# Kernel tuning notes

Measured on AMD Instinct MI355X. Metric: run time of the kernel, lower is better.

Reference implementation:

```python
import jax, jax.numpy as jnp
import numpy as np

N_NODES = 256
IN_FEATURES = 4096
OUT_FEATURES = 7
LAYERS = 4
WIRES = 8                      # ceil(log2(n_nodes))
DIM = 2 ** WIRES               # state-vector length = 256
P2 = WIRES * (WIRES - 1) // 2  # 28 controlled gates per block
N_W = 6 * WIRES + 3 * P2       # 132 weights per layer (matches weight_shape)
CPLX = jnp.complex64
# op2_all_layers ordering: gaps 1..w-1, then j
PAIRS = [(j, j + gap) for gap in range(1, WIRES) for j in range(WIRES - gap)]


def _ry(t):
    c, s = jnp.cos(t / 2), jnp.sin(t / 2)
    return jnp.stack([jnp.stack([c, -s]), jnp.stack([s, c])]).astype(CPLX)


def _rx(t):
    c = jnp.cos(t / 2).astype(CPLX)
    s = (-1j * jnp.sin(t / 2)).astype(CPLX)
    return jnp.stack([jnp.stack([c, s]), jnp.stack([s, c])])


def _rz(t):
    z = jnp.zeros((), CPLX)
    return jnp.stack([jnp.stack([jnp.exp(-0.5j * t).astype(CPLX), z]),
                      jnp.stack([z, jnp.exp(0.5j * t).astype(CPLX)])])


# Constant-angle gates (the source passes the integer weight index as the
# controlled-rotation angle, so these are compile-time numpy constants).
def _ry_np(a):
    c, s = np.cos(a / 2), np.sin(a / 2)
    return np.array([[c, -s], [s, c]], np.complex64)


def _rx_np(a):
    c, s = np.cos(a / 2), np.sin(a / 2)
    return np.array([[c, -1j * s], [-1j * s, c]], np.complex64)


def _rz_np(a):
    return np.diag([np.exp(-0.5j * a), np.exp(0.5j * a)]).astype(np.complex64)


def apply_1q(state, M, q):
    # state: [B] + [2]*WIRES; wire q lives on axis q+1 (wire 0 = MSB, PennyLane order)
    s = jnp.moveaxis(state, q + 1, -1)
    s = jnp.einsum('...b,ab->...a', s, M)
    return jnp.moveaxis(s, -1, q + 1)


def apply_c1q(state, M, c, t):
    # controlled gate: apply M on target wire t in the control==1 subspace
    s = jnp.moveaxis(state, (c + 1, t + 1), (-2, -1))
    s1 = jnp.einsum('...b,ab->...a', s[..., 1, :], M)
    s = jnp.stack([s[..., 0, :], s1], axis=-2)
    return jnp.moveaxis(s, (-2, -1), (c + 1, t + 1))


def q_layer(state, wv):
    # Faithful port of the source q_layer, including the quirk that the
    # CRY/CRX/CRZ angles are the integer running weight index (constants).
    wi = 0
    for q in range(WIRES):
        state = apply_1q(state, _ry(wv[wi + q]), q)
    wi += WIRES
    for i, (c, t) in enumerate(PAIRS):
        state = apply_c1q(state, _ry_np(float(wi + i)), c, t)
    wi += P2
    for q in range(WIRES):
        state = apply_1q(state, _ry(wv[wi + q]), q)
    wi += WIRES
    for q in range(WIRES):
        state = apply_1q(state, _rx(wv[wi + q]), q)
    wi += WIRES
    for i, (c, t) in enumerate(PAIRS):
        state = apply_c1q(state, _rx_np(float(wi + i)), c, t)
    wi += P2
    for q in range(WIRES):
        state = apply_1q(state, _rx(wv[wi + q]), q)
    wi += WIRES
    for q in range(WIRES):
        state = apply_1q(state, _rz(wv[wi + q]), q)
    wi += WIRES
    for i, (c, t) in enumerate(PAIRS):
        state = apply_c1q(state, _rz_np(float(wi + i)), c, t)
    wi += P2
    for q in range(WIRES):
        state = apply_1q(state, _rz(wv[wi + q]), q)
    return state


def circuit(samples, qweights):
    # samples: [B, N_NODES] real -> AmplitudeEmbedding(pad_with=0, normalize=True)
    B = samples.shape[0]
    v = samples
    if DIM > N_NODES:
        v = jnp.pad(v, ((0, 0), (0, DIM - N_NODES)))
    v = v / jnp.linalg.norm(v, axis=1, keepdims=True)
    state = v.astype(CPLX).reshape((B,) + (2,) * WIRES)
    layer = jax.checkpoint(q_layer)  # bounds residual memory under AD
    for l in range(LAYERS):
        state = layer(state, qweights[l])
    p = state.real ** 2 + state.imag ** 2  # probabilities, [B] + [2]*WIRES
    zs = []
    for q in range(WIRES):
        axes = tuple(a for a in range(1, WIRES + 1) if a != q + 1)
        m = p.sum(axis=axes)            # [B, 2]
        zs.append(m[:, 0] - m[:, 1])    # <Z_q> = P(0) - P(1)
    return jnp.stack(zs, axis=1)        # [B, WIRES]


def setup_inputs() -> dict:
    key = jax.random.key(0)
    k1, k2, k3, k4 = jax.random.split(key, 4)
    x = jax.random.normal(k1, (N_NODES, IN_FEATURES), jnp.float32)
    qweights = jax.random.uniform(k2, (LAYERS, N_W), jnp.float32, 0.0, 2.0 * np.pi)
    fc_w = jax.random.normal(k3, (OUT_FEATURES, WIRES), jnp.float32) / np.sqrt(WIRES)
    fc_b = jax.random.normal(k4, (OUT_FEATURES,), jnp.float32) / np.sqrt(WIRES)
    return {"x": x, "qweights": qweights, "fc_w": fc_w, "fc_b": fc_b}


def reference(x, qweights, fc_w, fc_b):
    z = circuit(x.T, qweights)      # [IN_FEATURES, WIRES]
    return z @ fc_w.T + fc_b        # [IN_FEATURES, OUT_FEATURES]
```

## Files before the change

kernel.cpp:

```cpp
#include <hip/hip_runtime.h>
#include <math.h>


namespace {

constexpr int NSAMP = 4096;
constexpr int NW_L  = 132;

constexpr double PI_D   = 3.14159265358979323846264338327950288;
constexpr double TWO_PI = 6.28318530717958647692528676655900577;

constexpr double red_pm_pi(double x) {
  double k = x / TWO_PI;
  long long ki = (long long)k;
  double r = x - (double)ki * TWO_PI;
  if (r > PI_D)  r -= TWO_PI;
  if (r < -PI_D) r += TWO_PI;
  return r;
}
constexpr double csin(double x) {
  double r = red_pm_pi(x), r2 = r * r, term = r, sum = r;
  for (int n = 1; n <= 13; ++n) { term *= -r2 / (double)((2*n)*(2*n+1)); sum += term; }
  return sum;
}
constexpr double ccos(double x) {
  double r = red_pm_pi(x), r2 = r * r, term = 1.0, sum = 1.0;
  for (int n = 1; n <= 13; ++n) { term *= -r2 / (double)((2*n-1)*(2*n)); sum += term; }
  return sum;
}

constexpr int PC[28] = {0,1,2,3,4,5,6, 0,1,2,3,4,5, 0,1,2,3,4, 0,1,2,3, 0,1,2, 0,1, 0};
constexpr int PT[28] = {1,2,3,4,5,6,7, 2,3,4,5,6,7, 3,4,5,6,7, 4,5,6,7, 5,6,7, 6,7, 7};

struct Tbl28 { float c[28]; float s[28]; };
constexpr Tbl28 mk_tbl(int base) {
  Tbl28 t{};
  for (int i = 0; i < 28; ++i) {
    double a = 0.5 * (double)(base + i);
    t.c[i] = (float)ccos(a);
    t.s[i] = (float)csin(a);
  }
  return t;
}
constexpr Tbl28 T_CRY = mk_tbl(8);
constexpr Tbl28 T_CRX = mk_tbl(52);

struct DTbl { float v[512]; };
constexpr DTbl mk_dcrz() {
  DTbl t{};
  for (int s = 0; s < 256; ++s) {
    double psi = 0.0;
    for (int i = 0; i < 28; ++i) {
      const int pc = 7 - PC[i], pt = 7 - PT[i];
      if ((s >> pc) & 1) {
        const double half = 0.5 * (double)(96 + i);
        psi += ((s >> pt) & 1) ? half : -half;
      }
    }
    t.v[2*s]   = (float)ccos(psi);
    t.v[2*s+1] = (float)csin(psi);
  }
  return t;
}
__device__ constexpr DTbl D_CRZ = mk_dcrz();

__device__ __forceinline__ float shx1(float v, int p) {
  if (p == 0) {
    int r = __builtin_amdgcn_update_dpp((int)__float_as_uint(v), (int)__float_as_uint(v),
                                        0xB1, 0xF, 0xF, true);
    return __uint_as_float((unsigned)r);
  }
  if (p == 1) {
    int r = __builtin_amdgcn_update_dpp((int)__float_as_uint(v), (int)__float_as_uint(v),
                                        0x4E, 0xF, 0xF, true);
    return __uint_as_float((unsigned)r);
  }
  if (p == 2) return __uint_as_float((unsigned)__builtin_amdgcn_ds_swizzle(
                      (int)__float_as_uint(v), 0x101F));
  if (p == 3) return __uint_as_float((unsigned)__builtin_amdgcn_ds_swizzle(
                      (int)__float_as_uint(v), 0x201F));
  if (p == 4) return __uint_as_float((unsigned)__builtin_amdgcn_ds_swizzle(
                      (int)__float_as_uint(v), 0x401F));
  return __shfl_xor(v, 32, 64);
}

__device__ __forceinline__ void gen_lane(float& ar, float& ai, int s, int p,
                                         float m00r, float m00i, float m01r, float m01i) {
  const int b = (s >> p) & 1;
  const float dr = m00r;
  const float di = b ? -m00i : m00i;
  const float g  = b ? -m01r : m01r;
  const float hh = m01i;
  const float pr = shx1(ar, p);
  const float pi = shx1(ai, p);
  const float mr = ar, mi = ai;
  ar = dr*mr - di*mi + g*pr - hh*pi;
  ai = dr*mi + di*mr + g*pi + hh*pr;
}
__device__ __forceinline__ void gen_xw(float& ar, float& ai, int s, int p,
                                       float m00r, float m00i, float m01r, float m01i,
                                       float2* xbuf) {
  xbuf[s] = make_float2(ar, ai);
  __syncthreads();
  const float2 pt = xbuf[s ^ (1 << p)];
  __syncthreads();
  const int b = (s >> p) & 1;
  const float dr = m00r;
  const float di = b ? -m00i : m00i;
  const float g  = b ? -m01r : m01r;
  const float hh = m01i;
  const float mr = ar, mi = ai;
  ar = dr*mr - di*mi + g*pt.x - hh*pt.y;
  ai = dr*mi + di*mr + g*pt.y + hh*pt.x;
}
__device__ __forceinline__ void cry_lane(float& ar, float& ai, int s, int pc, int pt,
                                         float cc, float sc) {
  const int ctrl = (s >> pc) & 1;
  const float ce = ctrl ? cc : 1.0f;
  float se = ((s >> pt) & 1) ? sc : -sc;
  se = ctrl ? se : 0.0f;
  const float pr = shx1(ar, pt);
  const float pi = shx1(ai, pt);
  ar = ce*ar + se*pr;
  ai = ce*ai + se*pi;
}
__device__ __forceinline__ void cry_xw(float& ar, float& ai, int s, int pc, int pt,
                                       float cc, float sc, float2* xbuf) {
  xbuf[s] = make_float2(ar, ai);
  __syncthreads();
  const float2 p = xbuf[s ^ (1 << pt)];
  __syncthreads();
  const int ctrl = (s >> pc) & 1;
  const float ce = ctrl ? cc : 1.0f;
  float se = ((s >> pt) & 1) ? sc : -sc;
  se = ctrl ? se : 0.0f;
  ar = ce*ar + se*p.x;
  ai = ce*ai + se*p.y;
}
__device__ __forceinline__ void crx_lane(float& ar, float& ai, int s, int pc, int pt,
                                         float cc, float sc) {
  const int ctrl = (s >> pc) & 1;
  const float ce = ctrl ? cc : 1.0f;
  const float se = ctrl ? sc : 0.0f;
  const float pr = shx1(ar, pt);
  const float pi = shx1(ai, pt);
  ar = ce*ar + se*pi;
  ai = ce*ai - se*pr;
}
__device__ __forceinline__ void crx_xw(float& ar, float& ai, int s, int pc, int pt,
                                       float cc, float sc, float2* xbuf) {
  xbuf[s] = make_float2(ar, ai);
  __syncthreads();
  const float2 p = xbuf[s ^ (1 << pt)];
  __syncthreads();
  const int ctrl = (s >> pc) & 1;
  const float ce = ctrl ? cc : 1.0f;
  const float se = ctrl ? sc : 0.0f;
  ar = ce*ar + se*p.y;
  ai = ce*ai - se*p.x;
}

__device__ __forceinline__ unsigned short f2bf(float f) {
  unsigned int u = __float_as_uint(f);
  u = (u + 0x7FFFu + ((u >> 16) & 1u)) >> 16;
  return (unsigned short)u;
}

typedef __attribute__((ext_vector_type(8))) short bf16x8;
typedef __attribute__((ext_vector_type(4))) float f32x4;

}

__global__ __launch_bounds__(256) void build_half4w(const float* __restrict__ qw,
                                                    float* __restrict__ U1c,
                                                    float* __restrict__ U2c) {
  __shared__ float4 sM[48];
  __shared__ float2 xbuf[256];
  const int tid = threadIdx.x;
  const int h   = blockIdx.x >> 8;
  const int s0  = blockIdx.x & 255;
  const int s   = tid;

  if (tid < 48) {
    const int lp  = tid / 24;
    const int rem = tid - lp * 24;
    const int j   = rem >> 3;
    const int q   = rem & 7;
    const int l   = 2 * h + lp;
    float a, bb;
    if (j == 0) {
      a  = qw[l * NW_L + q];
      bb = (l > 0) ? qw[(l - 1) * NW_L + 124 + q] : 0.f;
    } else if (j == 1) {
      a  = qw[l * NW_L + 44 + q];
      bb = qw[l * NW_L + 36 + q];
    } else {
      a  = (l < 3) ? qw[l * NW_L + 88 + q] : 0.f;
      bb = qw[l * NW_L + 80 + q];
    }
    float sa, ca, sb, cb;
    __sincosf(0.5f * a,  &sa, &ca);
    __sincosf(0.5f * bb, &sb, &cb);
    float4 m;
    if (j == 0)      m = make_float4(ca*cb, -ca*sb, -sa*cb, -sa*sb);
    else if (j == 1) m = make_float4(ca*cb, -sa*sb, -ca*sb, -sa*cb);
    else             m = make_float4(ca*cb, -sa*cb, -sb*sa, -sb*ca);
    sM[tid] = m;
  }

  float ar = (s == s0) ? 1.f : 0.f;
  float ai = 0.f;
  const float dzr = D_CRZ.v[2*s];
  const float dzi = D_CRZ.v[2*s+1];
  __syncthreads();

#pragma unroll 1
  for (int lp = 0; lp < 2; ++lp) {
    const int base = lp * 24;
#pragma unroll
    for (int q = 0; q < 8; ++q) {
      float4 m = sM[base + q];
      if (q == 0)      gen_xw(ar, ai, s, 7, m.x, m.y, m.z, m.w, xbuf);
      else if (q == 1) gen_xw(ar, ai, s, 6, m.x, m.y, m.z, m.w, xbuf);
      else             gen_lane(ar, ai, s, 7 - q, m.x, m.y, m.z, m.w);
    }
#pragma unroll
    for (int i = 0; i < 28; ++i) {
      const int pc = 7 - PC[i], pt = 7 - PT[i];
      const float cc = T_CRY.c[i], sc = T_CRY.s[i];
      if (pt == 6) cry_xw(ar, ai, s, pc, pt, cc, sc, xbuf);
      else         cry_lane(ar, ai, s, pc, pt, cc, sc);
    }
#pragma unroll
    for (int q = 0; q < 8; ++q) {
      float4 m = sM[base + 8 + q];
      if (q == 0)      gen_xw(ar, ai, s, 7, m.x, m.y, m.z, m.w, xbuf);
      else if (q == 1) gen_xw(ar, ai, s, 6, m.x, m.y, m.z, m.w, xbuf);
      else             gen_lane(ar, ai, s, 7 - q, m.x, m.y, m.z, m.w);
    }
#pragma unroll
    for (int i = 0; i < 28; ++i) {
      const int pc = 7 - PC[i], pt = 7 - PT[i];
      const float cc = T_CRX.c[i], sc = T_CRX.s[i];
      if (pt == 6) crx_xw(ar, ai, s, pc, pt, cc, sc, xbuf);
      else         crx_lane(ar, ai, s, pc, pt, cc, sc);
    }
#pragma unroll
    for (int q = 0; q < 8; ++q) {
      float4 m = sM[base + 16 + q];
      if (q == 0)      gen_xw(ar, ai, s, 7, m.x, m.y, m.z, m.w, xbuf);
      else if (q == 1) gen_xw(ar, ai, s, 6, m.x, m.y, m.z, m.w, xbuf);
      else             gen_lane(ar, ai, s, 7 - q, m.x, m.y, m.z, m.w);
    }
    if (2 * h + lp < 3) {
      const float mr = ar, mi = ai;
      ar = mr*dzr - mi*dzi;
      ai = mr*dzi + mi*dzr;
    }
  }

  float* Uc = h ? U2c : U1c;
  ((float2*)(Uc + (size_t)s0 * 512))[s] = make_float2(ar, ai);
}

__global__ __launch_bounds__(256) void combine_u(const float* __restrict__ U1c,
                                                 const float* __restrict__ U2c,
                                                 unsigned short* __restrict__ Ubf) {
  __shared__ float2 S2[32 * 16];
  __shared__ float2 S1[16 * 33];
  const int tid = threadIdx.x;
  const int ti  = tid & 15;
  const int tj  = tid >> 4;
  const int bi  = blockIdx.x & 15;
  const int bj  = blockIdx.x >> 4;

  float accr = 0.f, acci = 0.f;
#pragma unroll 1
  for (int kt = 0; kt < 8; ++kt) {
    __syncthreads();
#pragma unroll
    for (int v = 0; v < 2; ++v) {
      const int s = v * 256 + tid;
      const int k  = s >> 4, i = s & 15;
      S2[k * 16 + i] = *(const float2*)(U2c + (size_t)(kt*32 + k) * 512 + (bi*16 + i) * 2);
      const int j2 = s >> 5, k2 = s & 31;
      S1[j2 * 33 + k2] = *(const float2*)(U1c + (size_t)(bj*16 + j2) * 512 + (kt*32 + k2) * 2);
    }
    __syncthreads();
#pragma unroll
    for (int kk = 0; kk < 32; ++kk) {
      const float2 a = S2[kk * 16 + ti];
      const float2 b = S1[tj * 33 + kk];
      accr = fmaf(a.x, b.x, accr);  accr = fmaf(-a.y, b.y, accr);
      acci = fmaf(a.x, b.y, acci);  acci = fmaf(a.y, b.x, acci);
    }
  }
  const int i = bi * 16 + ti, j = bj * 16 + tj;
  Ubf[(size_t)i * 256 + j]         = f2bf(accr);
  Ubf[(size_t)(i + 256) * 256 + j] = f2bf(acci);
}

__global__ __launch_bounds__(1024) void eval3(const float* __restrict__ x,
                                              const unsigned short* __restrict__ Ubf,
                                              const float* __restrict__ fcw,
                                              const float* __restrict__ fcb,
                                              float* __restrict__ out) {
  __shared__ unsigned short Xs[16 * 264];
  __shared__ float Zp[16][16][9];
  __shared__ float Zf[16][9];
  const int tid  = threadIdx.x;
  const int lane = tid & 63;
  const int w    = tid >> 6;
  const int colbase = blockIdx.x * 16;

  {
    const int k  = tid >> 2;
    const int c4 = (tid & 3) * 4;
    const float4 v = *(const float4*)(x + (size_t)k * NSAMP + colbase + c4);
    Xs[(c4 + 0) * 264 + k] = f2bf(v.x);
    Xs[(c4 + 1) * 264 + k] = f2bf(v.y);
    Xs[(c4 + 2) * 264 + k] = f2bf(v.z);
    Xs[(c4 + 3) * 264 + k] = f2bf(v.w);
  }
  __syncthreads();

  const int quad = lane >> 4;
  const int n    = lane & 15;
  const int rowb = w * 32;

  f32x4 acc[2];
  acc[0] = (f32x4){0.f, 0.f, 0.f, 0.f};
  acc[1] = (f32x4){0.f, 0.f, 0.f, 0.f};

#pragma unroll
  for (int kt = 0; kt < 8; ++kt) {
    const bf16x8 bfrag = *(const bf16x8*)&Xs[n * 264 + kt * 32 + quad * 8];
#pragma unroll
    for (int rt = 0; rt < 2; ++rt) {
      const int row = rowb + rt * 16 + n;
      const bf16x8 afrag = *(const bf16x8*)(Ubf + (size_t)row * 256 + kt * 32 + quad * 8);
      acc[rt] = __builtin_amdgcn_mfma_f32_16x16x32_bf16(afrag, bfrag, acc[rt], 0, 0, 0);
    }
  }

  float za[9];
#pragma unroll
  for (int i = 0; i < 9; ++i) za[i] = 0.f;
  const float m4 = (lane & 32) ? -1.f : 1.f;
  const float m5 = (lane & 16) ? -1.f : 1.f;
#pragma unroll
  for (int rt = 0; rt < 2; ++rt) {
#pragma unroll
    for (int reg = 0; reg < 4; ++reg) {
      const float v = acc[rt][reg];
      const float p = v * v;
      za[0] += p;
      za[1] += (w & 4)   ? -p : p;
      za[2] += (w & 2)   ? -p : p;
      za[3] += (w & 1)   ? -p : p;
      za[4] += rt        ? -p : p;
      za[5] = fmaf(m4, p, za[5]);
      za[6] = fmaf(m5, p, za[6]);
      za[7] += (reg & 2) ? -p : p;
      za[8] += (reg & 1) ? -p : p;
    }
  }
#pragma unroll
  for (int off = 16; off <= 32; off <<= 1) {
#pragma unroll
    for (int i = 0; i < 9; ++i) za[i] += __shfl_xor(za[i], off, 64);
  }
  if (lane < 16) {
#pragma unroll
    for (int i = 0; i < 9; ++i) Zp[w][lane][i] = za[i];
  }
  __syncthreads();

  if (tid < 144) {
    const int col = tid / 9, q = tid - col * 9;
    float z = 0.f;
#pragma unroll
    for (int ww = 0; ww < 16; ++ww) z += Zp[ww][col][q];
    Zf[col][q] = z;
  }
  __syncthreads();

  if (tid < 112) {
    const int col = tid / 7, oo = tid - col * 7;
    const float inv = 1.f / Zf[col][0];
    float v = fcb[oo];
#pragma unroll
    for (int q = 0; q < 8; ++q)
      v = fmaf(fcw[oo * 8 + q], Zf[col][1 + q] * inv, v);
    out[(size_t)(colbase + col) * 7 + oo] = v;
  }
}

extern "C" void kernel_launch(void* const* d_in, const int* in_sizes, int n_in,
                              void* d_out, int out_size, void* d_ws, size_t ws_size,
                              hipStream_t stream) {
  const float* x   = (const float*)d_in[0];
  const float* qw  = (const float*)d_in[1];
  const float* fcw = (const float*)d_in[2];
  const float* fcb = (const float*)d_in[3];
  float* out = (float*)d_out;

  float* U1c = (float*)d_ws;
  float* U2c = U1c + 256 * 512;
  unsigned short* Ubf = (unsigned short*)(U2c + 256 * 512);

  hipLaunchKernelGGL(build_half4w, dim3(512), dim3(256),  0, stream, qw, U1c, U2c);
  hipLaunchKernelGGL(combine_u,    dim3(256), dim3(256),  0, stream, U1c, U2c, Ubf);
  hipLaunchKernelGGL(eval3,        dim3(256), dim3(1024), 0, stream, x, Ubf, fcw, fcb, out);
}
```

Before: 89.28 us.

## Drop unitary-combine kernel by chaining two half-circuit GEMMs in eval

Instead of forming the full circuit unitary with a separate complex matmul kernel, the build kernel now produces rows of each half-circuit directly, using an inverse-circuit trick to get rows instead of columns, and writes them in bf16 as a real-packed complex matrix. The eval kernel then applies the first half via MFMA, stages the bf16 intermediate in shared memory, and applies the second half as a 512x512 real block GEMM. This removes one kernel launch and the fp32 combine pass, at the cost of roughly three times the MFMA work per eval block and an extra bf16 rounding of the intermediate state.

```diff
diff --git a/kernel.cpp b/kernel.cpp
--- a/kernel.cpp
+++ b/kernel.cpp
@@ -171,14 +171,14 @@
 
 }
 
-__global__ __launch_bounds__(256) void build_half4w(const float* __restrict__ qw,
-                                                    float* __restrict__ U1c,
-                                                    float* __restrict__ U2c) {
+__global__ __launch_bounds__(256) void build_rows4w(const float* __restrict__ qw,
+                                                    unsigned short* __restrict__ U1bf,
+                                                    unsigned short* __restrict__ W2bf) {
   __shared__ float4 sM[48];
   __shared__ float2 xbuf[256];
   const int tid = threadIdx.x;
   const int h   = blockIdx.x >> 8;
-  const int s0  = blockIdx.x & 255;
+  const int o   = blockIdx.x & 255;
   const int s   = tid;
 
   if (tid < 48) {
@@ -208,104 +208,78 @@
     sM[tid] = m;
   }
 
-  float ar = (s == s0) ? 1.f : 0.f;
+  float ar = (s == o) ? 1.f : 0.f;
   float ai = 0.f;
-  const float dzr = D_CRZ.v[2*s];
-  const float dzi = D_CRZ.v[2*s+1];
+  const float dzr =  D_CRZ.v[2*s];
+  const float dzi = -D_CRZ.v[2*s+1];
   __syncthreads();
 
 #pragma unroll 1
-  for (int lp = 0; lp < 2; ++lp) {
+  for (int lp = 1; lp >= 0; --lp) {
+    const int l    = 2 * h + lp;
     const int base = lp * 24;
-#pragma unroll
-    for (int q = 0; q < 8; ++q) {
-      float4 m = sM[base + q];
-      if (q == 0)      gen_xw(ar, ai, s, 7, m.x, m.y, m.z, m.w, xbuf);
-      else if (q == 1) gen_xw(ar, ai, s, 6, m.x, m.y, m.z, m.w, xbuf);
-      else             gen_lane(ar, ai, s, 7 - q, m.x, m.y, m.z, m.w);
-    }
-#pragma unroll
-    for (int i = 0; i < 28; ++i) {
-      const int pc = 7 - PC[i], pt = 7 - PT[i];
-      const float cc = T_CRY.c[i], sc = T_CRY.s[i];
-      if (pt == 6) cry_xw(ar, ai, s, pc, pt, cc, sc, xbuf);
-      else         cry_lane(ar, ai, s, pc, pt, cc, sc);
-    }
-#pragma unroll
-    for (int q = 0; q < 8; ++q) {
-      float4 m = sM[base + 8 + q];
-      if (q == 0)      gen_xw(ar, ai, s, 7, m.x, m.y, m.z, m.w, xbuf);
-      else if (q == 1) gen_xw(ar, ai, s, 6, m.x, m.y, m.z, m.w, xbuf);
-      else             gen_lane(ar, ai, s, 7 - q, m.x, m.y, m.z, m.w);
-    }
-#pragma unroll
-    for (int i = 0; i < 28; ++i) {
-      const int pc = 7 - PC[i], pt = 7 - PT[i];
-      const float cc = T_CRX.c[i], sc = T_CRX.s[i];
-      if (pt == 6) crx_xw(ar, ai, s, pc, pt, cc, sc, xbuf);
-      else         crx_lane(ar, ai, s, pc, pt, cc, sc);
-    }
-#pragma unroll
-    for (int q = 0; q < 8; ++q) {
-      float4 m = sM[base + 16 + q];
-      if (q == 0)      gen_xw(ar, ai, s, 7, m.x, m.y, m.z, m.w, xbuf);
-      else if (q == 1) gen_xw(ar, ai, s, 6, m.x, m.y, m.z, m.w, xbuf);
-      else             gen_lane(ar, ai, s, 7 - q, m.x, m.y, m.z, m.w);
-    }
-    if (2 * h + lp < 3) {
+    if (l < 3) {
       const float mr = ar, mi = ai;
       ar = mr*dzr - mi*dzi;
       ai = mr*dzi + mi*dzr;
     }
-  }
-
-  float* Uc = h ? U2c : U1c;
-  ((float2*)(Uc + (size_t)s0 * 512))[s] = make_float2(ar, ai);
-}
-
-__global__ __launch_bounds__(256) void combine_u(const float* __restrict__ U1c,
-                                                 const float* __restrict__ U2c,
-                                                 unsigned short* __restrict__ Ubf) {
-  __shared__ float2 S2[32 * 16];
-  __shared__ float2 S1[16 * 33];
-  const int tid = threadIdx.x;
-  const int ti  = tid & 15;
-  const int tj  = tid >> 4;
-  const int bi  = blockIdx.x & 15;
-  const int bj  = blockIdx.x >> 4;
-
-  float accr = 0.f, acci = 0.f;
-#pragma unroll 1
-  for (int kt = 0; kt < 8; ++kt) {
-    __syncthreads();
-#pragma unroll
-    for (int v = 0; v < 2; ++v) {
-      const int s = v * 256 + tid;
-      const int k  = s >> 4, i = s & 15;
-      S2[k * 16 + i] = *(const float2*)(U2c + (size_t)(kt*32 + k) * 512 + (bi*16 + i) * 2);
-      const int j2 = s >> 5, k2 = s & 31;
-      S1[j2 * 33 + k2] = *(const float2*)(U1c + (size_t)(bj*16 + j2) * 512 + (kt*32 + k2) * 2);
-    }
-    __syncthreads();
-#pragma unroll
-    for (int kk = 0; kk < 32; ++kk) {
-      const float2 a = S2[kk * 16 + ti];
-      const float2 b = S1[tj * 33 + kk];
-      accr = fmaf(a.x, b.x, accr);  accr = fmaf(-a.y, b.y, accr);
-      acci = fmaf(a.x, b.y, acci);  acci = fmaf(a.y, b.x, acci);
-    }
-  }
-  const int i = bi * 16 + ti, j = bj * 16 + tj;
-  Ubf[(size_t)i * 256 + j]         = f2bf(accr);
-  Ubf[(size_t)(i + 256) * 256 + j] = f2bf(acci);
-}
-
-__global__ __launch_bounds__(1024) void eval3(const float* __restrict__ x,
-                                              const unsigned short* __restrict__ Ubf,
-                                              const float* __restrict__ fcw,
-                                              const float* __restrict__ fcb,
-                                              float* __restrict__ out) {
+#pragma unroll
+    for (int q = 0; q < 8; ++q) {
+      float4 m = sM[base + 16 + q];
+      if (q == 0)      gen_xw(ar, ai, s, 7, m.x, -m.y, -m.z, -m.w, xbuf);
+      else if (q == 1) gen_xw(ar, ai, s, 6, m.x, -m.y, -m.z, -m.w, xbuf);
+      else             gen_lane(ar, ai, s, 7 - q, m.x, -m.y, -m.z, -m.w);
+    }
+#pragma unroll
+    for (int i = 27; i >= 0; --i) {
+      const int pc = 7 - PC[i], pt = 7 - PT[i];
+      const float cc = T_CRX.c[i], sc = -T_CRX.s[i];
+      if (pt == 6) crx_xw(ar, ai, s, pc, pt, cc, sc, xbuf);
+      else         crx_lane(ar, ai, s, pc, pt, cc, sc);
+    }
+#pragma unroll
+    for (int q = 0; q < 8; ++q) {
+      float4 m = sM[base + 8 + q];
+      if (q == 0)      gen_xw(ar, ai, s, 7, m.x, -m.y, -m.z, -m.w, xbuf);
+      else if (q == 1) gen_xw(ar, ai, s, 6, m.x, -m.y, -m.z, -m.w, xbuf);
+      else             gen_lane(ar, ai, s, 7 - q, m.x, -m.y, -m.z, -m.w);
+    }
+#pragma unroll
+    for (int i = 27; i >= 0; --i) {
+      const int pc = 7 - PC[i], pt = 7 - PT[i];
+      const float cc = T_CRY.c[i], sc = -T_CRY.s[i];
+      if (pt == 6) cry_xw(ar, ai, s, pc, pt, cc, sc, xbuf);
+      else         cry_lane(ar, ai, s, pc, pt, cc, sc);
+    }
+#pragma unroll
+    for (int q = 0; q < 8; ++q) {
+      float4 m = sM[base + q];
+      if (q == 0)      gen_xw(ar, ai, s, 7, m.x, -m.y, -m.z, -m.w, xbuf);
+      else if (q == 1) gen_xw(ar, ai, s, 6, m.x, -m.y, -m.z, -m.w, xbuf);
+      else             gen_lane(ar, ai, s, 7 - q, m.x, -m.y, -m.z, -m.w);
+    }
+  }
+
+  if (h == 0) {
+    U1bf[(size_t)o * 256 + s]         = f2bf(ar);
+    U1bf[(size_t)(o + 256) * 256 + s] = f2bf(-ai);
+  } else {
+    U1bf += 0;
+    W2bf[(size_t)o * 512 + s]               = f2bf(ar);
+    W2bf[(size_t)o * 512 + 256 + s]         = f2bf(ai);
+    W2bf[(size_t)(o + 256) * 512 + s]       = f2bf(-ai);
+    W2bf[(size_t)(o + 256) * 512 + 256 + s] = f2bf(ar);
+  }
+}
+
+__global__ __launch_bounds__(1024) void eval_chain(const float* __restrict__ x,
+                                                   const unsigned short* __restrict__ U1bf,
+                                                   const unsigned short* __restrict__ W2bf,
+                                                   const float* __restrict__ fcw,
+                                                   const float* __restrict__ fcb,
+                                                   float* __restrict__ out) {
   __shared__ unsigned short Xs[16 * 264];
+  __shared__ unsigned short Ys[16 * 520];
   __shared__ float Zp[16][16][9];
   __shared__ float Zf[16][9];
   const int tid  = threadIdx.x;
@@ -328,17 +302,40 @@
   const int n    = lane & 15;
   const int rowb = w * 32;
 
+  {
+    f32x4 a1[2];
+    a1[0] = (f32x4){0.f, 0.f, 0.f, 0.f};
+    a1[1] = (f32x4){0.f, 0.f, 0.f, 0.f};
+#pragma unroll
+    for (int kt = 0; kt < 8; ++kt) {
+      const bf16x8 bfrag = *(const bf16x8*)&Xs[n * 264 + kt * 32 + quad * 8];
+#pragma unroll
+      for (int rt = 0; rt < 2; ++rt) {
+        const int row = rowb + rt * 16 + n;
+        const bf16x8 afrag = *(const bf16x8*)(U1bf + (size_t)row * 256 + kt * 32 + quad * 8);
+        a1[rt] = __builtin_amdgcn_mfma_f32_16x16x32_bf16(afrag, bfrag, a1[rt], 0, 0, 0);
+      }
+    }
+#pragma unroll
+    for (int rt = 0; rt < 2; ++rt) {
+      unsigned short p4[4];
+#pragma unroll
+      for (int reg = 0; reg < 4; ++reg) p4[reg] = f2bf(a1[rt][reg]);
+      *(uint2*)&Ys[n * 520 + rowb + rt * 16 + quad * 4] = *(const uint2*)p4;
+    }
+  }
+  __syncthreads();
+
   f32x4 acc[2];
   acc[0] = (f32x4){0.f, 0.f, 0.f, 0.f};
   acc[1] = (f32x4){0.f, 0.f, 0.f, 0.f};
-
-#pragma unroll
-  for (int kt = 0; kt < 8; ++kt) {
-    const bf16x8 bfrag = *(const bf16x8*)&Xs[n * 264 + kt * 32 + quad * 8];
+#pragma unroll
+  for (int kt = 0; kt < 16; ++kt) {
+    const bf16x8 bfrag = *(const bf16x8*)&Ys[n * 520 + kt * 32 + quad * 8];
 #pragma unroll
     for (int rt = 0; rt < 2; ++rt) {
       const int row = rowb + rt * 16 + n;
-      const bf16x8 afrag = *(const bf16x8*)(Ubf + (size_t)row * 256 + kt * 32 + quad * 8);
+      const bf16x8 afrag = *(const bf16x8*)(W2bf + (size_t)row * 512 + kt * 32 + quad * 8);
       acc[rt] = __builtin_amdgcn_mfma_f32_16x16x32_bf16(afrag, bfrag, acc[rt], 0, 0, 0);
     }
   }
@@ -405,11 +402,10 @@
   const float* fcb = (const float*)d_in[3];
   float* out = (float*)d_out;
 
-  float* U1c = (float*)d_ws;
-  float* U2c = U1c + 256 * 512;
-  unsigned short* Ubf = (unsigned short*)(U2c + 256 * 512);
-
-  hipLaunchKernelGGL(build_half4w, dim3(512), dim3(256),  0, stream, qw, U1c, U2c);
-  hipLaunchKernelGGL(combine_u,    dim3(256), dim3(256),  0, stream, U1c, U2c, Ubf);
-  hipLaunchKernelGGL(eval3,        dim3(256), dim3(1024), 0, stream, x, Ubf, fcw, fcb, out);
-}
+  unsigned short* U1bf = (unsigned short*)d_ws;
+  unsigned short* W2bf = U1bf + (size_t)512 * 256;
+
+  hipLaunchKernelGGL(build_rows4w, dim3(512), dim3(256),  0, stream, qw, U1bf, W2bf);
+  hipLaunchKernelGGL(eval_chain,   dim3(256), dim3(1024), 0, stream,
+                     x, U1bf, W2bf, fcw, fcb, out);
+}
```

Measured after the change: 94.60 us. +6.0%, slower.

## Split unitary build into per-layer quarters and chain two GEMMs in eval

Applied to the files above, without the earlier changes.

The circuit unitary is now built one layer per block, across four times as many blocks with half the serial gate depth each. The combine kernel now forms two two-layer products, U1 = L1·L0 and U2 = L3·L2, instead of one four-layer product. U1 is stored as a stacked real/imag bf16 matrix, and U2 as a 512x512 real-block matrix [[Re,-Im],[Im,Re]]. The eval kernel then does two chained MFMA GEMMs (U1·x, then W2·y) with the intermediate in shared memory. This shortens the serial critical path of the build stage, at the cost of more eval-stage MFMA work, roughly tripling its matmul FLOPs, and an extra bf16 rounding of the intermediate state.

```diff
diff --git a/kernel.cpp b/kernel.cpp
--- a/kernel.cpp
+++ b/kernel.cpp
@@ -169,24 +169,50 @@
 typedef __attribute__((ext_vector_type(8))) short bf16x8;
 typedef __attribute__((ext_vector_type(4))) float f32x4;
 
-}
-
-__global__ __launch_bounds__(256) void build_half4w(const float* __restrict__ qw,
-                                                    float* __restrict__ U1c,
-                                                    float* __restrict__ U2c) {
-  __shared__ float4 sM[48];
+__device__ __forceinline__ void cgemm_tile(const float* __restrict__ bufA,
+                                           const float* __restrict__ bufB,
+                                           int bi, int bj, int tid,
+                                           float& accr, float& acci,
+                                           float2* S2 , float2* S1 ) {
+  const int ti = tid & 15;
+  const int tj = tid >> 4;
+  accr = 0.f; acci = 0.f;
+#pragma unroll 1
+  for (int kt = 0; kt < 8; ++kt) {
+    __syncthreads();
+#pragma unroll
+    for (int v = 0; v < 2; ++v) {
+      const int s = v * 256 + tid;
+      const int k = s >> 4, i = s & 15;
+      S2[k * 16 + i] = *(const float2*)(bufA + (size_t)(kt*32 + k) * 512 + (bi*16 + i) * 2);
+      const int j2 = s >> 5, k2 = s & 31;
+      S1[j2 * 33 + k2] = *(const float2*)(bufB + (size_t)(bj*16 + j2) * 512 + (kt*32 + k2) * 2);
+    }
+    __syncthreads();
+#pragma unroll
+    for (int kk = 0; kk < 32; ++kk) {
+      const float2 a = S2[kk * 16 + ti];
+      const float2 b = S1[tj * 33 + kk];
+      accr = fmaf(a.x, b.x, accr);  accr = fmaf(-a.y, b.y, accr);
+      acci = fmaf(a.x, b.y, acci);  acci = fmaf(a.y, b.x, acci);
+    }
+  }
+}
+
+}
+
+__global__ __launch_bounds__(256) void build_quarter4w(const float* __restrict__ qw,
+                                                       float* __restrict__ Uq) {
+  __shared__ float4 sM[24];
   __shared__ float2 xbuf[256];
   const int tid = threadIdx.x;
-  const int h   = blockIdx.x >> 8;
+  const int l   = blockIdx.x >> 8;
   const int s0  = blockIdx.x & 255;
   const int s   = tid;
 
-  if (tid < 48) {
-    const int lp  = tid / 24;
-    const int rem = tid - lp * 24;
-    const int j   = rem >> 3;
-    const int q   = rem & 7;
-    const int l   = 2 * h + lp;
+  if (tid < 24) {
+    const int j = tid >> 3;
+    const int q = tid & 7;
     float a, bb;
     if (j == 0) {
       a  = qw[l * NW_L + q];
@@ -214,98 +240,105 @@
   const float dzi = D_CRZ.v[2*s+1];
   __syncthreads();
 
-#pragma unroll 1
-  for (int lp = 0; lp < 2; ++lp) {
-    const int base = lp * 24;
-#pragma unroll
-    for (int q = 0; q < 8; ++q) {
-      float4 m = sM[base + q];
-      if (q == 0)      gen_xw(ar, ai, s, 7, m.x, m.y, m.z, m.w, xbuf);
-      else if (q == 1) gen_xw(ar, ai, s, 6, m.x, m.y, m.z, m.w, xbuf);
-      else             gen_lane(ar, ai, s, 7 - q, m.x, m.y, m.z, m.w);
-    }
-#pragma unroll
-    for (int i = 0; i < 28; ++i) {
-      const int pc = 7 - PC[i], pt = 7 - PT[i];
-      const float cc = T_CRY.c[i], sc = T_CRY.s[i];
-      if (pt == 6) cry_xw(ar, ai, s, pc, pt, cc, sc, xbuf);
-      else         cry_lane(ar, ai, s, pc, pt, cc, sc);
-    }
-#pragma unroll
-    for (int q = 0; q < 8; ++q) {
-      float4 m = sM[base + 8 + q];
-      if (q == 0)      gen_xw(ar, ai, s, 7, m.x, m.y, m.z, m.w, xbuf);
-      else if (q == 1) gen_xw(ar, ai, s, 6, m.x, m.y, m.z, m.w, xbuf);
-      else             gen_lane(ar, ai, s, 7 - q, m.x, m.y, m.z, m.w);
-    }
-#pragma unroll
-    for (int i = 0; i < 28; ++i) {
-      const int pc = 7 - PC[i], pt = 7 - PT[i];
-      const float cc = T_CRX.c[i], sc = T_CRX.s[i];
-      if (pt == 6) crx_xw(ar, ai, s, pc, pt, cc, sc, xbuf);
-      else         crx_lane(ar, ai, s, pc, pt, cc, sc);
-    }
-#pragma unroll
-    for (int q = 0; q < 8; ++q) {
-      float4 m = sM[base + 16 + q];
-      if (q == 0)      gen_xw(ar, ai, s, 7, m.x, m.y, m.z, m.w, xbuf);
-      else if (q == 1) gen_xw(ar, ai, s, 6, m.x, m.y, m.z, m.w, xbuf);
-      else             gen_lane(ar, ai, s, 7 - q, m.x, m.y, m.z, m.w);
-    }
-    if (2 * h + lp < 3) {
-      const float mr = ar, mi = ai;
-      ar = mr*dzr - mi*dzi;
-      ai = mr*dzi + mi*dzr;
-    }
-  }
-
-  float* Uc = h ? U2c : U1c;
-  ((float2*)(Uc + (size_t)s0 * 512))[s] = make_float2(ar, ai);
-}
-
-__global__ __launch_bounds__(256) void combine_u(const float* __restrict__ U1c,
-                                                 const float* __restrict__ U2c,
-                                                 unsigned short* __restrict__ Ubf) {
+#pragma unroll
+  for (int q = 0; q < 8; ++q) {
+    float4 m = sM[q];
+    if (q == 0)      gen_xw(ar, ai, s, 7, m.x, m.y, m.z, m.w, xbuf);
+    else if (q == 1) gen_xw(ar, ai, s, 6, m.x, m.y, m.z, m.w, xbuf);
+    else             gen_lane(ar, ai, s, 7 - q, m.x, m.y, m.z, m.w);
+  }
+#pragma unroll
+  for (int i = 0; i < 28; ++i) {
+    const int pc = 7 - PC[i], pt = 7 - PT[i];
+    const float cc = T_CRY.c[i], sc = T_CRY.s[i];
+    if (pt == 6) cry_xw(ar, ai, s, pc, pt, cc, sc, xbuf);
+    else         cry_lane(ar, ai, s, pc, pt, cc, sc);
+  }
+#pragma unroll
+  for (int q = 0; q < 8; ++q) {
+    float4 m = sM[8 + q];
+    if (q == 0)      gen_xw(ar, ai, s, 7, m.x, m.y, m.z, m.w, xbuf);
+    else if (q == 1) gen_xw(ar, ai, s, 6, m.x, m.y, m.z, m.w, xbuf);
+    else             gen_lane(ar, ai, s, 7 - q, m.x, m.y, m.z, m.w);
+  }
+#pragma unroll
+  for (int i = 0; i < 28; ++i) {
+    const int pc = 7 - PC[i], pt = 7 - PT[i];
+    const float cc = T_CRX.c[i], sc = T_CRX.s[i];
+    if (pt == 6) crx_xw(ar, ai, s, pc, pt, cc, sc, xbuf);
+    else         crx_lane(ar, ai, s, pc, pt, cc, sc);
+  }
+#pragma unroll
+  for (int q = 0; q < 8; ++q) {
+    float4 m = sM[16 + q];
+    if (q == 0)      gen_xw(ar, ai, s, 7, m.x, m.y, m.z, m.w, xbuf);
+    else if (q == 1) gen_xw(ar, ai, s, 6, m.x, m.y, m.z, m.w, xbuf);
+    else             gen_lane(ar, ai, s, 7 - q, m.x, m.y, m.z, m.w);
+  }
+  if (l < 3) {
+    const float mr = ar, mi = ai;
+    ar = mr*dzr - mi*dzi;
+    ai = mr*dzi + mi*dzr;
+  }
+
+  ((float2*)(Uq + (size_t)(l * 256 + s0) * 512))[s] = make_float2(ar, ai);
+}
+
+__global__ __launch_bounds__(256) void combine_emit(const float* __restrict__ Uq,
+                                                    unsigned short* __restrict__ U1bf,
+                                                    unsigned short* __restrict__ W2bf) {
   __shared__ float2 S2[32 * 16];
   __shared__ float2 S1[16 * 33];
+  __shared__ float Tre[16][17];
+  __shared__ float Tim[16][17];
   const int tid = threadIdx.x;
-  const int ti  = tid & 15;
-  const int tj  = tid >> 4;
-  const int bi  = blockIdx.x & 15;
-  const int bj  = blockIdx.x >> 4;
-
-  float accr = 0.f, acci = 0.f;
-#pragma unroll 1
-  for (int kt = 0; kt < 8; ++kt) {
-    __syncthreads();
-#pragma unroll
-    for (int v = 0; v < 2; ++v) {
-      const int s = v * 256 + tid;
-      const int k  = s >> 4, i = s & 15;
-      S2[k * 16 + i] = *(const float2*)(U2c + (size_t)(kt*32 + k) * 512 + (bi*16 + i) * 2);
-      const int j2 = s >> 5, k2 = s & 31;
-      S1[j2 * 33 + k2] = *(const float2*)(U1c + (size_t)(bj*16 + j2) * 512 + (kt*32 + k2) * 2);
-    }
-    __syncthreads();
-#pragma unroll
-    for (int kk = 0; kk < 32; ++kk) {
-      const float2 a = S2[kk * 16 + ti];
-      const float2 b = S1[tj * 33 + kk];
-      accr = fmaf(a.x, b.x, accr);  accr = fmaf(-a.y, b.y, accr);
-      acci = fmaf(a.x, b.y, acci);  acci = fmaf(a.y, b.x, acci);
-    }
-  }
-  const int i = bi * 16 + ti, j = bj * 16 + tj;
-  Ubf[(size_t)i * 256 + j]         = f2bf(accr);
-  Ubf[(size_t)(i + 256) * 256 + j] = f2bf(acci);
-}
-
-__global__ __launch_bounds__(1024) void eval3(const float* __restrict__ x,
-                                              const unsigned short* __restrict__ Ubf,
-                                              const float* __restrict__ fcw,
-                                              const float* __restrict__ fcb,
-                                              float* __restrict__ out) {
+  const int p   = blockIdx.x >> 8;
+  const int rem = blockIdx.x & 255;
+  const int bi  = rem & 15;
+  const int bj  = rem >> 4;
+  const float* bufA = Uq + (size_t)(2*p + 1) * 256 * 512;
+  const float* bufB = Uq + (size_t)(2*p) * 256 * 512;
+
+  float accr, acci;
+  cgemm_tile(bufA, bufB, bi, bj, tid, accr, acci, S2, S1);
+
+  Tre[tid & 15][tid >> 4] = accr;
+  Tim[tid & 15][tid >> 4] = acci;
+  __syncthreads();
+
+  const int part = tid >> 6;
+  const int rr   = (tid & 63) >> 2;
+  const int cg   = tid & 3;
+  unsigned short pk[4];
+  if (p == 0) {
+    if (part < 2) {
+#pragma unroll
+      for (int k = 0; k < 4; ++k)
+        pk[k] = f2bf(part ? Tim[rr][cg*4 + k] : Tre[rr][cg*4 + k]);
+      const int row = bi * 16 + rr + part * 256;
+      *(uint2*)(U1bf + (size_t)row * 256 + bj * 16 + cg * 4) = *(const uint2*)pk;
+    }
+  } else {
+#pragma unroll
+    for (int k = 0; k < 4; ++k) {
+      const float v = (part == 0 || part == 3) ? Tre[rr][cg*4 + k]
+                    : (part == 1 ? -Tim[rr][cg*4 + k] : Tim[rr][cg*4 + k]);
+      pk[k] = f2bf(v);
+    }
+    const int row = bi * 16 + rr + ((part >= 2) ? 256 : 0);
+    const int col = bj * 16 + cg * 4 + ((part & 1) ? 256 : 0);
+    *(uint2*)(W2bf + (size_t)row * 512 + col) = *(const uint2*)pk;
+  }
+}
+
+__global__ __launch_bounds__(1024) void eval_chain(const float* __restrict__ x,
+                                                   const unsigned short* __restrict__ U1bf,
+                                                   const unsigned short* __restrict__ W2bf,
+                                                   const float* __restrict__ fcw,
+                                                   const float* __restrict__ fcb,
+                                                   float* __restrict__ out) {
   __shared__ unsigned short Xs[16 * 264];
+  __shared__ unsigned short Ys[16 * 520];
   __shared__ float Zp[16][16][9];
   __shared__ float Zf[16][9];
   const int tid  = threadIdx.x;
@@ -328,17 +361,40 @@
   const int n    = lane & 15;
   const int rowb = w * 32;
 
+  {
+    f32x4 a1[2];
+    a1[0] = (f32x4){0.f, 0.f, 0.f, 0.f};
+    a1[1] = (f32x4){0.f, 0.f, 0.f, 0.f};
+#pragma unroll
+    for (int kt = 0; kt < 8; ++kt) {
+      const bf16x8 bfrag = *(const bf16x8*)&Xs[n * 264 + kt * 32 + quad * 8];
+#pragma unroll
+      for (int rt = 0; rt < 2; ++rt) {
+        const int row = rowb + rt * 16 + n;
+        const bf16x8 afrag = *(const bf16x8*)(U1bf + (size_t)row * 256 + kt * 32 + quad * 8);
+        a1[rt] = __builtin_amdgcn_mfma_f32_16x16x32_bf16(afrag, bfrag, a1[rt], 0, 0, 0);
+      }
+    }
+#pragma unroll
+    for (int rt = 0; rt < 2; ++rt) {
+      unsigned short p4[4];
+#pragma unroll
+      for (int reg = 0; reg < 4; ++reg) p4[reg] = f2bf(a1[rt][reg]);
+      *(uint2*)&Ys[n * 520 + rowb + rt * 16 + quad * 4] = *(const uint2*)p4;
+    }
+  }
+  __syncthreads();
+
   f32x4 acc[2];
   acc[0] = (f32x4){0.f, 0.f, 0.f, 0.f};
   acc[1] = (f32x4){0.f, 0.f, 0.f, 0.f};
-
-#pragma unroll
-  for (int kt = 0; kt < 8; ++kt) {
-    const bf16x8 bfrag = *(const bf16x8*)&Xs[n * 264 + kt * 32 + quad * 8];
+#pragma unroll
+  for (int kt = 0; kt < 16; ++kt) {
+    const bf16x8 bfrag = *(const bf16x8*)&Ys[n * 520 + kt * 32 + quad * 8];
 #pragma unroll
     for (int rt = 0; rt < 2; ++rt) {
       const int row = rowb + rt * 16 + n;
-      const bf16x8 afrag = *(const bf16x8*)(Ubf + (size_t)row * 256 + kt * 32 + quad * 8);
+      const bf16x8 afrag = *(const bf16x8*)(W2bf + (size_t)row * 512 + kt * 32 + quad * 8);
       acc[rt] = __builtin_amdgcn_mfma_f32_16x16x32_bf16(afrag, bfrag, acc[rt], 0, 0, 0);
     }
   }
@@ -405,11 +461,12 @@
   const float* fcb = (const float*)d_in[3];
   float* out = (float*)d_out;
 
-  float* U1c = (float*)d_ws;
-  float* U2c = U1c + 256 * 512;
-  unsigned short* Ubf = (unsigned short*)(U2c + 256 * 512);
-
-  hipLaunchKernelGGL(build_half4w, dim3(512), dim3(256),  0, stream, qw, U1c, U2c);
-  hipLaunchKernelGGL(combine_u,    dim3(256), dim3(256),  0, stream, U1c, U2c, Ubf);
-  hipLaunchKernelGGL(eval3,        dim3(256), dim3(1024), 0, stream, x, Ubf, fcw, fcb, out);
-}
+  float* Uq = (float*)d_ws;
+  unsigned short* U1bf = (unsigned short*)(Uq + (size_t)4 * 256 * 512);
+  unsigned short* W2bf = U1bf + (size_t)512 * 256;
+
+  hipLaunchKernelGGL(build_quarter4w, dim3(1024), dim3(256),  0, stream, qw, Uq);
+  hipLaunchKernelGGL(combine_emit,    dim3(512),  dim3(256),  0, stream, Uq, U1bf, W2bf);
+  hipLaunchKernelGGL(eval_chain,      dim3(256),  dim3(1024), 0, stream,
+                     x, U1bf, W2bf, fcw, fcb, out);
+}
```

After: 105.6 us. 1.18x slower.

## Fuse cross-wave gates into precomputed 4x4 two-qubit blocks to cut barriers

Applied to the files above, without the earlier changes.

The unitary-building kernel previously moved amplitudes through shared memory with two barriers for every gate on the two top wires (bits 7 and 6), which cross wavefronts. It now precomputes, per block section, a 4x4 matrix fusing the two top-wire single-qubit gates with the first controlled rotation on that pair. Each section then applies that matrix with one shared-memory exchange using double-buffered scratch and one barrier. The remaining gates stay as in-wave lane shuffles. This cuts many barriers in exchange for a small setup step and extra shared-memory reads per section.

```diff
diff --git a/kernel.cpp b/kernel.cpp
--- a/kernel.cpp
+++ b/kernel.cpp
@@ -97,22 +97,6 @@
   ar = dr*mr - di*mi + g*pr - hh*pi;
   ai = dr*mi + di*mr + g*pi + hh*pr;
 }
-__device__ __forceinline__ void gen_xw(float& ar, float& ai, int s, int p,
-                                       float m00r, float m00i, float m01r, float m01i,
-                                       float2* xbuf) {
-  xbuf[s] = make_float2(ar, ai);
-  __syncthreads();
-  const float2 pt = xbuf[s ^ (1 << p)];
-  __syncthreads();
-  const int b = (s >> p) & 1;
-  const float dr = m00r;
-  const float di = b ? -m00i : m00i;
-  const float g  = b ? -m01r : m01r;
-  const float hh = m01i;
-  const float mr = ar, mi = ai;
-  ar = dr*mr - di*mi + g*pt.x - hh*pt.y;
-  ai = dr*mi + di*mr + g*pt.y + hh*pt.x;
-}
 __device__ __forceinline__ void cry_lane(float& ar, float& ai, int s, int pc, int pt,
                                          float cc, float sc) {
   const int ctrl = (s >> pc) & 1;
@@ -124,19 +108,6 @@
   ar = ce*ar + se*pr;
   ai = ce*ai + se*pi;
 }
-__device__ __forceinline__ void cry_xw(float& ar, float& ai, int s, int pc, int pt,
-                                       float cc, float sc, float2* xbuf) {
-  xbuf[s] = make_float2(ar, ai);
-  __syncthreads();
-  const float2 p = xbuf[s ^ (1 << pt)];
-  __syncthreads();
-  const int ctrl = (s >> pc) & 1;
-  const float ce = ctrl ? cc : 1.0f;
-  float se = ((s >> pt) & 1) ? sc : -sc;
-  se = ctrl ? se : 0.0f;
-  ar = ce*ar + se*p.x;
-  ai = ce*ai + se*p.y;
-}
 __device__ __forceinline__ void crx_lane(float& ar, float& ai, int s, int pc, int pt,
                                          float cc, float sc) {
   const int ctrl = (s >> pc) & 1;
@@ -147,17 +118,10 @@
   ar = ce*ar + se*pi;
   ai = ce*ai - se*pr;
 }
-__device__ __forceinline__ void crx_xw(float& ar, float& ai, int s, int pc, int pt,
-                                       float cc, float sc, float2* xbuf) {
-  xbuf[s] = make_float2(ar, ai);
-  __syncthreads();
-  const float2 p = xbuf[s ^ (1 << pt)];
-  __syncthreads();
-  const int ctrl = (s >> pc) & 1;
-  const float ce = ctrl ? cc : 1.0f;
-  const float se = ctrl ? sc : 0.0f;
-  ar = ce*ar + se*p.y;
-  ai = ce*ai - se*p.x;
+
+__device__ __forceinline__ float2 mat2(float4 m, int r, int c) {
+  if (r == 0) return (c == 0) ? make_float2(m.x, m.y) : make_float2(m.z, m.w);
+  return (c == 0) ? make_float2(-m.z, m.w) : make_float2(m.x, -m.y);
 }
 
 __device__ __forceinline__ unsigned short f2bf(float f) {
@@ -171,11 +135,12 @@
 
 }
 
-__global__ __launch_bounds__(256) void build_half4w(const float* __restrict__ qw,
-                                                    float* __restrict__ U1c,
-                                                    float* __restrict__ U2c) {
+__global__ __launch_bounds__(256) void build_half4w_f(const float* __restrict__ qw,
+                                                      float* __restrict__ U1c,
+                                                      float* __restrict__ U2c) {
   __shared__ float4 sM[48];
-  __shared__ float2 xbuf[256];
+  __shared__ float2 sG[2][3][16];
+  __shared__ float2 xb[2][256];
   const int tid = threadIdx.x;
   const int h   = blockIdx.x >> 8;
   const int s0  = blockIdx.x & 255;
@@ -207,55 +172,89 @@
     else             m = make_float4(ca*cb, -sa*cb, -sb*sa, -sb*ca);
     sM[tid] = m;
   }
+  __syncthreads();
+
+  if (tid < 96) {
+    const int lp = tid / 48;
+    const int rm = tid - lp * 48;
+    const int mi = rm >> 4;
+    const int e  = rm & 15;
+    const int v  = e >> 2, u = e & 3;
+    const int a  = v >> 1, b = v & 1, ap = u >> 1, bp = u & 1;
+    const float4 A4 = sM[lp * 24 + mi * 8 + 0];
+    const float4 B4 = sM[lp * 24 + mi * 8 + 1];
+    const float2 A = mat2(A4, a, ap);
+    float2 Bv;
+    if (mi == 2 || a == 0) {
+      Bv = mat2(B4, b, bp);
+    } else {
+      const float2 B0 = mat2(B4, 0, bp);
+      const float2 B1 = mat2(B4, 1, bp);
+      if (mi == 0) {
+        const float c = T_CRY.c[0], sg = T_CRY.s[0];
+        Bv = (b == 0) ? make_float2(c*B0.x - sg*B1.x, c*B0.y - sg*B1.y)
+                      : make_float2(sg*B0.x + c*B1.x, sg*B0.y + c*B1.y);
+      } else {
+        const float c = T_CRX.c[0], sg = T_CRX.s[0];
+        Bv = (b == 0) ? make_float2(c*B0.x + sg*B1.y, c*B0.y - sg*B1.x)
+                      : make_float2(sg*B0.y + c*B1.x, -sg*B0.x + c*B1.y);
+      }
+    }
+    sG[lp][mi][e] = make_float2(A.x*Bv.x - A.y*Bv.y, A.x*Bv.y + A.y*Bv.x);
+  }
 
   float ar = (s == s0) ? 1.f : 0.f;
   float ai = 0.f;
   const float dzr = D_CRZ.v[2*s];
   const float dzi = D_CRZ.v[2*s+1];
+  const int v    = s >> 6;
+  const int slow = s & 63;
   __syncthreads();
 
+  int pb = 0;
 #pragma unroll 1
   for (int lp = 0; lp < 2; ++lp) {
     const int base = lp * 24;
-#pragma unroll
-    for (int q = 0; q < 8; ++q) {
-      float4 m = sM[base + q];
-      if (q == 0)      gen_xw(ar, ai, s, 7, m.x, m.y, m.z, m.w, xbuf);
-      else if (q == 1) gen_xw(ar, ai, s, 6, m.x, m.y, m.z, m.w, xbuf);
-      else             gen_lane(ar, ai, s, 7 - q, m.x, m.y, m.z, m.w);
-    }
-#pragma unroll
-    for (int i = 0; i < 28; ++i) {
-      const int pc = 7 - PC[i], pt = 7 - PT[i];
-      const float cc = T_CRY.c[i], sc = T_CRY.s[i];
-      if (pt == 6) cry_xw(ar, ai, s, pc, pt, cc, sc, xbuf);
-      else         cry_lane(ar, ai, s, pc, pt, cc, sc);
-    }
-#pragma unroll
-    for (int q = 0; q < 8; ++q) {
-      float4 m = sM[base + 8 + q];
-      if (q == 0)      gen_xw(ar, ai, s, 7, m.x, m.y, m.z, m.w, xbuf);
-      else if (q == 1) gen_xw(ar, ai, s, 6, m.x, m.y, m.z, m.w, xbuf);
-      else             gen_lane(ar, ai, s, 7 - q, m.x, m.y, m.z, m.w);
-    }
-#pragma unroll
-    for (int i = 0; i < 28; ++i) {
-      const int pc = 7 - PC[i], pt = 7 - PT[i];
-      const float cc = T_CRX.c[i], sc = T_CRX.s[i];
-      if (pt == 6) crx_xw(ar, ai, s, pc, pt, cc, sc, xbuf);
-      else         crx_lane(ar, ai, s, pc, pt, cc, sc);
-    }
-#pragma unroll
-    for (int q = 0; q < 8; ++q) {
-      float4 m = sM[base + 16 + q];
-      if (q == 0)      gen_xw(ar, ai, s, 7, m.x, m.y, m.z, m.w, xbuf);
-      else if (q == 1) gen_xw(ar, ai, s, 6, m.x, m.y, m.z, m.w, xbuf);
-      else             gen_lane(ar, ai, s, 7 - q, m.x, m.y, m.z, m.w);
+#pragma unroll 1
+    for (int mi = 0; mi < 3; ++mi) {
+      {
+        float2* buf = xb[pb];
+        buf[s] = make_float2(ar, ai);
+        __syncthreads();
+        float nr = 0.f, ni = 0.f;
+#pragma unroll
+        for (int u = 0; u < 4; ++u) {
+          const float2 g = sG[lp][mi][v * 4 + u];
+          const float2 p = buf[slow + 64 * u];
+          nr += g.x*p.x - g.y*p.y;
+          ni += g.x*p.y + g.y*p.x;
+        }
+        ar = nr; ai = ni;
+        pb ^= 1;
+      }
+#pragma unroll
+      for (int q = 2; q < 8; ++q) {
+        float4 m = sM[base + mi * 8 + q];
+        gen_lane(ar, ai, s, 7 - q, m.x, m.y, m.z, m.w);
+      }
+      if (mi == 0) {
+#pragma unroll
+        for (int i = 1; i < 28; ++i) {
+          const int pc = 7 - PC[i], pt = 7 - PT[i];
+          cry_lane(ar, ai, s, pc, pt, T_CRY.c[i], T_CRY.s[i]);
+        }
+      } else if (mi == 1) {
+#pragma unroll
+        for (int i = 1; i < 28; ++i) {
+          const int pc = 7 - PC[i], pt = 7 - PT[i];
+          crx_lane(ar, ai, s, pc, pt, T_CRX.c[i], T_CRX.s[i]);
+        }
+      }
     }
     if (2 * h + lp < 3) {
-      const float mr = ar, mi = ai;
-      ar = mr*dzr - mi*dzi;
-      ai = mr*dzi + mi*dzr;
+      const float mr = ar, mi2 = ai;
+      ar = mr*dzr - mi2*dzi;
+      ai = mr*dzi + mi2*dzr;
     }
   }
 
@@ -409,7 +408,7 @@
   float* U2c = U1c + 256 * 512;
   unsigned short* Ubf = (unsigned short*)(U2c + 256 * 512);
 
-  hipLaunchKernelGGL(build_half4w, dim3(512), dim3(256),  0, stream, qw, U1c, U2c);
-  hipLaunchKernelGGL(combine_u,    dim3(256), dim3(256),  0, stream, U1c, U2c, Ubf);
-  hipLaunchKernelGGL(eval3,        dim3(256), dim3(1024), 0, stream, x, Ubf, fcw, fcb, out);
-}
+  hipLaunchKernelGGL(build_half4w_f, dim3(512), dim3(256),  0, stream, qw, U1c, U2c);
+  hipLaunchKernelGGL(combine_u,      dim3(256), dim3(256),  0, stream, U1c, U2c, Ubf);
+  hipLaunchKernelGGL(eval3,          dim3(256), dim3(1024), 0, stream, x, Ubf, fcw, fcb, out);
+}
```

Measured after the change: 95.71 us. 7.2% more time.
